# Kernel tuning notes

Measured on AMD Instinct MI355X. Metric: run time of the kernel, lower is better.

Reference implementation:

```python
import jax, jax.numpy as jnp
import numpy as np

T, B, D, H, NQ = 2048, 512, 128, 128, 8

def setup_inputs() -> dict:
    key = jax.random.key(0)
    ks = jax.random.split(key, 9)
    s = 1.0 / np.sqrt(D + H)
    inp = {"inputs": jax.random.normal(ks[0], (T, B, D), dtype=jnp.float32)}
    names = ["Wf", "bf", "Wi", "bi", "Wu", "bu", "Wo", "bo"]
    for j, nm in enumerate(names):
        shp = (NQ, D + H) if nm.startswith("W") else (NQ,)
        inp[nm] = jax.random.normal(ks[j + 1], shp, dtype=jnp.float32) * s
    return inp


def _qgate(z):
    # Expected fraction of '1' outcomes after RX(theta_i)|0> on each wire:
    # P(1) = sin^2(theta/2); mean over wires -> one scalar per sample.
    # (Deterministic expectation in place of the 100-shot Aer sampling; the
    # appended random_circuit is unseeded/non-deterministic and is omitted.)
    return jnp.mean(jnp.sin(z * 0.5) ** 2, axis=-1)  # [B]


def reference(inputs, Wf, bf, Wi, bi, Wu, bu, Wo, bo):
    Bsz = inputs.shape[1]
    h0 = jnp.zeros((Bsz, H), dtype=inputs.dtype)
    c0 = jnp.zeros((Bsz, H), dtype=inputs.dtype)

    def step(carry, x):
        hx, cx = carry
        comb = jnp.concatenate([x, hx], axis=1)  # [B, D+H]
        f = jax.nn.sigmoid(_qgate(comb @ Wf.T + bf))[:, None]
        i = jax.nn.sigmoid(_qgate(comb @ Wi.T + bi))[:, None]
        g = jnp.tanh(_qgate(comb @ Wu.T + bu))[:, None]
        o = jax.nn.sigmoid(_qgate(comb @ Wo.T + bo))[:, None]
        cx = f * cx + i * g
        hx = o * jnp.tanh(cx)
        return (hx, cx), hx

    (hx, cx), stacked = jax.lax.scan(step, (h0, c0), inputs)
    return stacked, hx, cx
```

## Files before the change

### kernel.cpp

```cpp
#include <hip/hip_runtime.h>
#include <stdint.h>


typedef __attribute__((ext_vector_type(8))) short short8;
typedef __attribute__((ext_vector_type(4))) float float4v;

#define TSTEPS 2048
#define BATCH  512
#define DIMX   128
#define HID    128
#define ROWS   (TSTEPS * BATCH)

__device__ __forceinline__ float bf2f(unsigned short u) {
  union { unsigned int i; float f; } v; v.i = ((unsigned int)u) << 16; return v.f;
}
__device__ __forceinline__ unsigned short f2bf(float f) {
  union { float f; unsigned int i; } v; v.f = f;
  unsigned int u = v.i;
  return (unsigned short)((u + 0x7FFFu + ((u >> 16) & 1u)) >> 16);
}

__device__ __forceinline__ void split8(const float* __restrict__ p,
                                       short8& hi, short8& lo) {
  float4v a = *(const float4v*)p;
  float4v b = *(const float4v*)(p + 4);
#pragma unroll
  for (int j = 0; j < 8; ++j) {
    float x = (j < 4) ? a[j] : b[j - 4];
    unsigned short h = f2bf(x);
    float r = x - bf2f(h);
    hi[j] = (short)h;
    lo[j] = (short)f2bf(r);
  }
}

__global__ __launch_bounds__(256) void qlstm_gemm(
    const float* __restrict__ X,
    const float* __restrict__ Wf, const float* __restrict__ bfv,
    const float* __restrict__ Wi, const float* __restrict__ biv,
    const float* __restrict__ Wu, const float* __restrict__ buv,
    const float* __restrict__ Wo, const float* __restrict__ bov,
    _Float16* __restrict__ Z)
{
  const int lane = threadIdx.x & 63;
  const int wave = threadIdx.x >> 6;
  const int m    = lane & 15;
  const int quad = lane >> 4;
  const long row0 = ((long)blockIdx.x * 4 + wave) * 16;

  const int q = m & 7;
  const float* b0 = (m < 8) ? Wf : Wi;
  const float* b1 = (m < 8) ? Wu : Wo;

  short8 b0h[4], b0l[4], b1h[4], b1l[4];
#pragma unroll
  for (int ks = 0; ks < 4; ++ks) {
    split8(b0 + q * 256 + ks * 32 + quad * 8, b0h[ks], b0l[ks]);
    split8(b1 + q * 256 + ks * 32 + quad * 8, b1h[ks], b1l[ks]);
  }

  float4v acc0 = {0.f, 0.f, 0.f, 0.f};
  float4v acc1 = {0.f, 0.f, 0.f, 0.f};
  const float* xrow = X + (row0 + m) * DIMX;
#pragma unroll
  for (int ks = 0; ks < 4; ++ks) {
    short8 ah, al;
    split8(xrow + ks * 32 + quad * 8, ah, al);
    acc0 = __builtin_amdgcn_mfma_f32_16x16x32_bf16(ah, b0h[ks], acc0, 0, 0, 0);
    acc0 = __builtin_amdgcn_mfma_f32_16x16x32_bf16(al, b0h[ks], acc0, 0, 0, 0);
    acc0 = __builtin_amdgcn_mfma_f32_16x16x32_bf16(ah, b0l[ks], acc0, 0, 0, 0);
    acc1 = __builtin_amdgcn_mfma_f32_16x16x32_bf16(ah, b1h[ks], acc1, 0, 0, 0);
    acc1 = __builtin_amdgcn_mfma_f32_16x16x32_bf16(al, b1h[ks], acc1, 0, 0, 0);
    acc1 = __builtin_amdgcn_mfma_f32_16x16x32_bf16(ah, b1l[ks], acc1, 0, 0, 0);
  }

  const float INV2PI = 0.15915494309189535f;
  const float bias0 = ((m < 8) ? bfv : biv)[q];
  const float bias1 = ((m < 8) ? buv : bov)[q];
#pragma unroll
  for (int r = 0; r < 4; ++r) {
    long row = row0 + quad * 4 + r;
    float z0 = __builtin_amdgcn_fractf((acc0[r] + bias0) * INV2PI);
    float z1 = __builtin_amdgcn_fractf((acc1[r] + bias1) * INV2PI);
    Z[row * 32 + m]      = (_Float16)z0;
    Z[row * 32 + 16 + m] = (_Float16)z1;
  }
}

template <int CTRL>
__device__ __forceinline__ float dppf(float x) {
  return __int_as_float(
      __builtin_amdgcn_mov_dpp(__float_as_int(x), CTRL, 0xF, 0xF, true));
}

__global__ __launch_bounds__(64) void qlstm_scan(
    const _Float16* __restrict__ Z,
    const float* __restrict__ Wf, const float* __restrict__ Wi,
    const float* __restrict__ Wu, const float* __restrict__ Wo,
    float* __restrict__ out)
{
  const int lane = threadIdx.x;
  const int g32  = lane & 31;
  const int gate = g32 >> 3;
  const int q    = g32 & 7;
  const int b    = blockIdx.x * 2 + (lane >> 5);

  const float* Wsel = (gate == 0) ? Wf : (gate == 1) ? Wi
                    : (gate == 2) ? Wu : Wo;
  const float* wp = Wsel + q * 256 + 128;
  float ws = 0.f;
#pragma unroll 8
  for (int j = 0; j < 128; ++j) ws += wp[j];
  const float INV2PI = 0.15915494309189535f;
  const float wrev = ws * INV2PI;

  const float L2E = 1.4426950408889634f;
  const float ka = (gate == 2) ? (L2E / 8.f)  : (L2E / 16.f);
  const float kb = (gate == 2) ? (-L2E)       : (-0.5f * L2E);
  const float s2 = (gate == 2) ? 2.f : 1.f;
  const float s3 = (gate == 2) ? -1.f : 0.f;

  const int base32 = lane & 32;
  const int adr_f = (base32 + 0  + q) * 4;
  const int adr_i = (base32 + 8  + q) * 4;
  const int adr_u = (base32 + 16 + q) * 4;
  const int adr_o = (base32 + 24 + q) * 4;

  float c = 0.f, h = 0.f;

  const _Float16* zp = Z + (long)b * 32 + g32;
  _Float16 zr[8];
#pragma unroll
  for (int j = 0; j < 8; ++j) zr[j] = zp[(long)j * 16384];

  float* orow = out + (long)b * HID + g32 * 4;

  for (int tt = 0; tt < TSTEPS; tt += 8) {
#pragma unroll
    for (int j = 0; j < 8; ++j) {
      const int t = tt + j;
      float zx = (float)zr[j];
      int tn = t + 8; if (tn > TSTEPS - 1) tn = TSTEPS - 1;
      zr[j] = zp[(long)tn * 16384];

      float r  = __builtin_fmaf(h, wrev, zx);
      r        = __builtin_amdgcn_fractf(r);
      float cs = __builtin_amdgcn_cosf(r);

      float s = cs + dppf<0x141>(cs);
      s += dppf<0xB1>(s);
      s += dppf<0x4E>(s);

      float e = __builtin_amdgcn_exp2f(__builtin_fmaf(s, ka, kb));
      float v = __builtin_fmaf(__builtin_amdgcn_rcpf(1.f + e), s2, s3);

      float fg = __int_as_float(__builtin_amdgcn_ds_bpermute(adr_f, __float_as_int(v)));
      float ig = __int_as_float(__builtin_amdgcn_ds_bpermute(adr_i, __float_as_int(v)));
      float ug = __int_as_float(__builtin_amdgcn_ds_bpermute(adr_u, __float_as_int(v)));
      float og = __int_as_float(__builtin_amdgcn_ds_bpermute(adr_o, __float_as_int(v)));

      c = __builtin_fmaf(fg, c, ig * ug);
      float e2 = __builtin_amdgcn_exp2f(c * (2.f * L2E));
      float th = __builtin_fmaf(-2.f, __builtin_amdgcn_rcpf(1.f + e2), 1.f);
      h = og * th;

      float4v hv = {h, h, h, h};
      *(float4v*)(orow + (long)t * (BATCH * HID)) = hv;
    }
  }

  float4v hv = {h, h, h, h};
  float4v cv = {c, c, c, c};
  float* hxp = out + (long)TSTEPS * (BATCH * HID) + (long)b * HID + g32 * 4;
  *(float4v*)hxp = hv;
  *(float4v*)(hxp + BATCH * HID) = cv;
}

extern "C" void kernel_launch(void* const* d_in, const int* in_sizes, int n_in,
                              void* d_out, int out_size, void* d_ws, size_t ws_size,
                              hipStream_t stream) {
  (void)in_sizes; (void)n_in; (void)out_size; (void)ws_size;
  const float* X   = (const float*)d_in[0];
  const float* Wf  = (const float*)d_in[1];
  const float* bfv = (const float*)d_in[2];
  const float* Wi  = (const float*)d_in[3];
  const float* biv = (const float*)d_in[4];
  const float* Wu  = (const float*)d_in[5];
  const float* buv = (const float*)d_in[6];
  const float* Wo  = (const float*)d_in[7];
  const float* bov = (const float*)d_in[8];

  _Float16* Z = (_Float16*)d_ws;
  float* out = (float*)d_out;

  qlstm_gemm<<<ROWS / 64, 256, 0, stream>>>(X, Wf, bfv, Wi, biv, Wu, buv, Wo, bov, Z);
  qlstm_scan<<<BATCH / 2, 64, 0, stream>>>(Z, Wf, Wi, Wu, Wo, out);
}
```

Baseline: 1.167 ms.

## Fuse input projection GEMM into recurrent scan with LDS double buffering

```diff
diff --git a/kernel.cpp b/kernel.cpp
--- a/kernel.cpp
+++ b/kernel.cpp
@@ -9,83 +9,9 @@
 #define BATCH  512
 #define DIMX   128
 #define HID    128
-#define ROWS   (TSTEPS * BATCH)
-
-__device__ __forceinline__ float bf2f(unsigned short u) {
-  union { unsigned int i; float f; } v; v.i = ((unsigned int)u) << 16; return v.f;
-}
-__device__ __forceinline__ unsigned short f2bf(float f) {
-  union { float f; unsigned int i; } v; v.f = f;
-  unsigned int u = v.i;
-  return (unsigned short)((u + 0x7FFFu + ((u >> 16) & 1u)) >> 16);
-}
-
-__device__ __forceinline__ void split8(const float* __restrict__ p,
-                                       short8& hi, short8& lo) {
-  float4v a = *(const float4v*)p;
-  float4v b = *(const float4v*)(p + 4);
-#pragma unroll
-  for (int j = 0; j < 8; ++j) {
-    float x = (j < 4) ? a[j] : b[j - 4];
-    unsigned short h = f2bf(x);
-    float r = x - bf2f(h);
-    hi[j] = (short)h;
-    lo[j] = (short)f2bf(r);
-  }
-}
-
-__global__ __launch_bounds__(256) void qlstm_gemm(
-    const float* __restrict__ X,
-    const float* __restrict__ Wf, const float* __restrict__ bfv,
-    const float* __restrict__ Wi, const float* __restrict__ biv,
-    const float* __restrict__ Wu, const float* __restrict__ buv,
-    const float* __restrict__ Wo, const float* __restrict__ bov,
-    _Float16* __restrict__ Z)
-{
-  const int lane = threadIdx.x & 63;
-  const int wave = threadIdx.x >> 6;
-  const int m    = lane & 15;
-  const int quad = lane >> 4;
-  const long row0 = ((long)blockIdx.x * 4 + wave) * 16;
-
-  const int q = m & 7;
-  const float* b0 = (m < 8) ? Wf : Wi;
-  const float* b1 = (m < 8) ? Wu : Wo;
-
-  short8 b0h[4], b0l[4], b1h[4], b1l[4];
-#pragma unroll
-  for (int ks = 0; ks < 4; ++ks) {
-    split8(b0 + q * 256 + ks * 32 + quad * 8, b0h[ks], b0l[ks]);
-    split8(b1 + q * 256 + ks * 32 + quad * 8, b1h[ks], b1l[ks]);
-  }
-
-  float4v acc0 = {0.f, 0.f, 0.f, 0.f};
-  float4v acc1 = {0.f, 0.f, 0.f, 0.f};
-  const float* xrow = X + (row0 + m) * DIMX;
-#pragma unroll
-  for (int ks = 0; ks < 4; ++ks) {
-    short8 ah, al;
-    split8(xrow + ks * 32 + quad * 8, ah, al);
-    acc0 = __builtin_amdgcn_mfma_f32_16x16x32_bf16(ah, b0h[ks], acc0, 0, 0, 0);
-    acc0 = __builtin_amdgcn_mfma_f32_16x16x32_bf16(al, b0h[ks], acc0, 0, 0, 0);
-    acc0 = __builtin_amdgcn_mfma_f32_16x16x32_bf16(ah, b0l[ks], acc0, 0, 0, 0);
-    acc1 = __builtin_amdgcn_mfma_f32_16x16x32_bf16(ah, b1h[ks], acc1, 0, 0, 0);
-    acc1 = __builtin_amdgcn_mfma_f32_16x16x32_bf16(al, b1h[ks], acc1, 0, 0, 0);
-    acc1 = __builtin_amdgcn_mfma_f32_16x16x32_bf16(ah, b1l[ks], acc1, 0, 0, 0);
-  }
-
-  const float INV2PI = 0.15915494309189535f;
-  const float bias0 = ((m < 8) ? bfv : biv)[q];
-  const float bias1 = ((m < 8) ? buv : bov)[q];
-#pragma unroll
-  for (int r = 0; r < 4; ++r) {
-    long row = row0 + quad * 4 + r;
-    float z0 = __builtin_amdgcn_fractf((acc0[r] + bias0) * INV2PI);
-    float z1 = __builtin_amdgcn_fractf((acc1[r] + bias1) * INV2PI);
-    Z[row * 32 + m]      = (_Float16)z0;
-    Z[row * 32 + 16 + m] = (_Float16)z1;
-  }
-}
+#define TBLK   (TSTEPS / 8)
+#define LROW   33
+#define LBUF   (16 * LROW)
 
 template <int CTRL>
 __device__ __forceinline__ float dppf(float x) {
@@ -93,17 +19,51 @@
       __builtin_amdgcn_mov_dpp(__float_as_int(x), CTRL, 0xF, 0xF, true));
 }
 
-__global__ __launch_bounds__(64) void qlstm_scan(
-    const _Float16* __restrict__ Z,
-    const float* __restrict__ Wf, const float* __restrict__ Wi,
-    const float* __restrict__ Wu, const float* __restrict__ Wo,
+__device__ __forceinline__ void splitv(float4v a, float4v b,
+                                       short8& hi, short8& lo) {
+#pragma unroll
+  for (int j = 0; j < 8; ++j) {
+    float x = (j < 4) ? a[j] : b[j - 4];
+    unsigned int u = __float_as_uint(x);
+    float r = x - __uint_as_float(u & 0xFFFF0000u);
+    hi[j] = (short)(u >> 16);
+    lo[j] = (short)(__float_as_uint(r) >> 16);
+  }
+}
+
+__global__ __launch_bounds__(64) void qlstm_fused(
+    const float* __restrict__ X,
+    const float* __restrict__ Wf, const float* __restrict__ bfv,
+    const float* __restrict__ Wi, const float* __restrict__ biv,
+    const float* __restrict__ Wu, const float* __restrict__ buv,
+    const float* __restrict__ Wo, const float* __restrict__ bov,
     float* __restrict__ out)
 {
-  const int lane = threadIdx.x;
-  const int g32  = lane & 31;
-  const int gate = g32 >> 3;
-  const int q    = g32 & 7;
-  const int b    = blockIdx.x * 2 + (lane >> 5);
+  __shared__ float Zl[2 * LBUF];
+
+  const int lane  = threadIdx.x;
+  const int m     = lane & 15;
+  const int quad  = lane >> 4;
+  const int g32   = lane & 31;
+  const int gate  = g32 >> 3;
+  const int q     = g32 & 7;
+  const int bhalf = lane >> 5;
+  const int b0    = blockIdx.x * 2;
+
+  const int qm = m & 7;
+  const float* Bt0 = (m < 8) ? Wf : Wi;
+  const float* Bt1 = (m < 8) ? Wu : Wo;
+  short8 b0h[4], b0l[4], b1h[4], b1l[4];
+#pragma unroll
+  for (int ks = 0; ks < 4; ++ks) {
+    const float* p0 = Bt0 + qm * 256 + ks * 32 + quad * 8;
+    const float* p1 = Bt1 + qm * 256 + ks * 32 + quad * 8;
+    splitv(*(const float4v*)p0, *(const float4v*)(p0 + 4), b0h[ks], b0l[ks]);
+    splitv(*(const float4v*)p1, *(const float4v*)(p1 + 4), b1h[ks], b1l[ks]);
+  }
+  const float INV2PI = 0.15915494309189535f;
+  const float bias0 = ((m < 8) ? bfv : biv)[qm];
+  const float bias1 = ((m < 8) ? buv : bov)[qm];
 
   const float* Wsel = (gate == 0) ? Wf : (gate == 1) ? Wi
                     : (gate == 2) ? Wu : Wo;
@@ -111,12 +71,11 @@
   float ws = 0.f;
 #pragma unroll 8
   for (int j = 0; j < 128; ++j) ws += wp[j];
-  const float INV2PI = 0.15915494309189535f;
   const float wrev = ws * INV2PI;
 
   const float L2E = 1.4426950408889634f;
-  const float ka = (gate == 2) ? (L2E / 8.f)  : (L2E / 16.f);
-  const float kb = (gate == 2) ? (-L2E)       : (-0.5f * L2E);
+  const float ka = (gate == 2) ? (L2E / 8.f) : (L2E / 16.f);
+  const float kb = (gate == 2) ? (-L2E)      : (-0.5f * L2E);
   const float s2 = (gate == 2) ? 2.f : 1.f;
   const float s3 = (gate == 2) ? -1.f : 0.f;
 
@@ -126,25 +85,60 @@
   const int adr_u = (base32 + 16 + q) * 4;
   const int adr_o = (base32 + 24 + q) * 4;
 
+  const float* arow = X + ((long)(m >> 1) * BATCH + b0 + (m & 1)) * DIMX;
+  float4v Aa[8];
+
+#define LOADA(tb)                                                            \
+  {                                                                          \
+    const float* p_ = arow + (long)(tb) * (8 * BATCH * DIMX);                \
+    _Pragma("unroll")                                                        \
+    for (int ks_ = 0; ks_ < 4; ++ks_) {                                      \
+      Aa[2 * ks_]     = *(const float4v*)(p_ + ks_ * 32 + quad * 8);         \
+      Aa[2 * ks_ + 1] = *(const float4v*)(p_ + ks_ * 32 + quad * 8 + 4);     \
+    }                                                                        \
+  }
+
+#define PRODUCE(buf)                                                         \
+  {                                                                          \
+    float4v acc0 = {0.f, 0.f, 0.f, 0.f};                                     \
+    float4v acc1 = {0.f, 0.f, 0.f, 0.f};                                     \
+    _Pragma("unroll")                                                        \
+    for (int ks_ = 0; ks_ < 4; ++ks_) {                                      \
+      short8 ah_, al_;                                                       \
+      splitv(Aa[2 * ks_], Aa[2 * ks_ + 1], ah_, al_);                        \
+      acc0 = __builtin_amdgcn_mfma_f32_16x16x32_bf16(ah_, b0h[ks_], acc0, 0, 0, 0); \
+      acc0 = __builtin_amdgcn_mfma_f32_16x16x32_bf16(al_, b0h[ks_], acc0, 0, 0, 0); \
+      acc0 = __builtin_amdgcn_mfma_f32_16x16x32_bf16(ah_, b0l[ks_], acc0, 0, 0, 0); \
+      acc1 = __builtin_amdgcn_mfma_f32_16x16x32_bf16(ah_, b1h[ks_], acc1, 0, 0, 0); \
+      acc1 = __builtin_amdgcn_mfma_f32_16x16x32_bf16(al_, b1h[ks_], acc1, 0, 0, 0); \
+      acc1 = __builtin_amdgcn_mfma_f32_16x16x32_bf16(ah_, b1l[ks_], acc1, 0, 0, 0); \
+    }                                                                        \
+    _Pragma("unroll")                                                        \
+    for (int r_ = 0; r_ < 4; ++r_) {                                         \
+      int row_ = quad * 4 + r_;                                              \
+      Zl[(buf) * LBUF + row_ * LROW + m]      = (acc0[r_] + bias0) * INV2PI; \
+      Zl[(buf) * LBUF + row_ * LROW + m + 16] = (acc1[r_] + bias1) * INV2PI; \
+    }                                                                        \
+  }
+
   float c = 0.f, h = 0.f;
+  float* orow = out + (long)(b0 + bhalf) * HID + g32 * 4;
 
-  const _Float16* zp = Z + (long)b * 32 + g32;
-  _Float16 zr[8];
-#pragma unroll
-  for (int j = 0; j < 8; ++j) zr[j] = zp[(long)j * 16384];
+  LOADA(0);
+  PRODUCE(0);
+  LOADA(1);
 
-  float* orow = out + (long)b * HID + g32 * 4;
+  for (int k = 0; k < TBLK; ++k) {
+    PRODUCE((k + 1) & 1);
+    int kn = k + 2; if (kn > TBLK - 1) kn = TBLK - 1;
+    LOADA(kn);
 
-  for (int tt = 0; tt < TSTEPS; tt += 8) {
+    const float* zb = Zl + (k & 1) * LBUF + bhalf * LROW + g32;
 #pragma unroll
     for (int j = 0; j < 8; ++j) {
-      const int t = tt + j;
-      float zx = (float)zr[j];
-      int tn = t + 8; if (tn > TSTEPS - 1) tn = TSTEPS - 1;
-      zr[j] = zp[(long)tn * 16384];
+      float zx = zb[j * 2 * LROW];
 
       float r  = __builtin_fmaf(h, wrev, zx);
-      r        = __builtin_amdgcn_fractf(r);
       float cs = __builtin_amdgcn_cosf(r);
 
       float s = cs + dppf<0x141>(cs);
@@ -165,21 +159,24 @@
       h = og * th;
 
       float4v hv = {h, h, h, h};
-      *(float4v*)(orow + (long)t * (BATCH * HID)) = hv;
+      *(float4v*)orow = hv;
+      orow += (long)BATCH * HID;
     }
   }
 
   float4v hv = {h, h, h, h};
   float4v cv = {c, c, c, c};
-  float* hxp = out + (long)TSTEPS * (BATCH * HID) + (long)b * HID + g32 * 4;
+  float* hxp = out + (long)TSTEPS * BATCH * HID + (long)(b0 + bhalf) * HID + g32 * 4;
   *(float4v*)hxp = hv;
   *(float4v*)(hxp + BATCH * HID) = cv;
+#undef LOADA
+#undef PRODUCE
 }
 
 extern "C" void kernel_launch(void* const* d_in, const int* in_sizes, int n_in,
                               void* d_out, int out_size, void* d_ws, size_t ws_size,
                               hipStream_t stream) {
-  (void)in_sizes; (void)n_in; (void)out_size; (void)ws_size;
+  (void)in_sizes; (void)n_in; (void)out_size; (void)d_ws; (void)ws_size;
   const float* X   = (const float*)d_in[0];
   const float* Wf  = (const float*)d_in[1];
   const float* bfv = (const float*)d_in[2];
@@ -189,10 +186,7 @@
   const float* buv = (const float*)d_in[6];
   const float* Wo  = (const float*)d_in[7];
   const float* bov = (const float*)d_in[8];
-
-  _Float16* Z = (_Float16*)d_ws;
   float* out = (float*)d_out;
 
-  qlstm_gemm<<<ROWS / 64, 256, 0, stream>>>(X, Wf, bfv, Wi, biv, Wu, buv, Wo, bov, Z);
-  qlstm_scan<<<BATCH / 2, 64, 0, stream>>>(Z, Wf, Wi, Wu, Wo, out);
+  qlstm_fused<<<BATCH / 2, 64, 0, stream>>>(X, Wf, bfv, Wi, biv, Wu, buv, Wo, bov, out);
 }
```

Result: faster. 993.0 us (-14.9%).
